# Kernel tuning notes

Measured on AMD Instinct MI355X. Metric: run time of the kernel, lower is better.

Reference implementation:

```python
import jax, jax.numpy as jnp
import numpy as np

EMB = 384
HEADS = 6
QDIM = 64
DFF = 4 * EMB
EPS = 1e-5


def layer_norm(x, g, b):
    mu = jnp.mean(x, axis=-1, keepdims=True)
    var = jnp.mean((x - mu) ** 2, axis=-1, keepdims=True)
    return (x - mu) * jax.lax.rsqrt(var + EPS) * g + b


def setup_inputs() -> dict:
    key = jax.random.key(0)
    ks = jax.random.split(key, 12)
    s = EMB ** -0.5
    return {
        "x": jax.random.normal(ks[0], (32, 512, EMB), dtype=jnp.float32),
        "Wq": jax.random.normal(ks[1], (EMB, EMB), dtype=jnp.float32) * s,
        "Wk": jax.random.normal(ks[2], (EMB, EMB), dtype=jnp.float32) * s,
        "Wv": jax.random.normal(ks[3], (EMB, EMB), dtype=jnp.float32) * s,
        "Wp": jax.random.normal(ks[4], (EMB, EMB), dtype=jnp.float32) * s,
        "bp": jnp.zeros((EMB,), dtype=jnp.float32),
        "g1": jnp.ones((EMB,), dtype=jnp.float32),
        "b1": jnp.zeros((EMB,), dtype=jnp.float32),
        "g2": jnp.ones((EMB,), dtype=jnp.float32),
        "b2": jnp.zeros((EMB,), dtype=jnp.float32),
        "W1": jax.random.normal(ks[5], (EMB, DFF), dtype=jnp.float32) * s,
        "bf1": jnp.zeros((DFF,), dtype=jnp.float32),
        "W2": jax.random.normal(ks[6], (DFF, EMB), dtype=jnp.float32) * (DFF ** -0.5),
        "bf2": jnp.zeros((EMB,), dtype=jnp.float32),
    }


def reference(x, Wq, Wk, Wv, Wp, bp, g1, b1, g2, b2, W1, bf1, W2, bf2):
    B, T, C = x.shape
    # --- self-attention on ln1(x) ---
    h = layer_norm(x, g1, b1)
    q = (h @ Wq).reshape(B, T, HEADS, QDIM).transpose(0, 2, 1, 3)  # [B,H,T,D]
    k = (h @ Wk).reshape(B, T, HEADS, QDIM).transpose(0, 2, 1, 3)
    v = (h @ Wv).reshape(B, T, HEADS, QDIM).transpose(0, 2, 1, 3)
    aff = jnp.einsum('bhtd,bhsd->bhts', q, k) * (QDIM ** -0.5)  # [B,H,T,T]
    causal = jnp.tril(jnp.ones((T, T), dtype=bool))
    aff = jnp.where(causal, aff, -jnp.inf)
    aff = jax.nn.softmax(aff, axis=-1)
    o = jnp.einsum('bhts,bhsd->bhtd', aff, v)
    o = o.transpose(0, 2, 1, 3).reshape(B, T, C)
    x = x + (o @ Wp + bp)
    # --- feed-forward on ln2(x) ---
    h2 = layer_norm(x, g2, b2)
    ff = jax.nn.relu(h2 @ W1 + bf1) @ W2 + bf2
    return x + ff
```

## Files before the change

kernel.cpp:

```cpp
#include <hip/hip_runtime.h>
#include <cstdint>
#include <cstddef>

#define DEVINL __device__ __forceinline__

typedef short short8 __attribute__((ext_vector_type(8)));
typedef float f32x4 __attribute__((ext_vector_type(4)));
typedef unsigned short ushort;
typedef ushort u16x8 __attribute__((ext_vector_type(8)));
typedef ushort u16x4 __attribute__((ext_vector_type(4)));

DEVINL float bf2f(ushort u) {
  union { unsigned int i; float f; } v; v.i = ((unsigned int)u) << 16; return v.f;
}
DEVINL ushort f2bf(float f) {
  union { float f; unsigned int i; } v; v.f = f;
  unsigned int u = v.i;
  unsigned int r = u + 0x7fffu + ((u >> 16) & 1u);
  return (ushort)(r >> 16);
}

DEVINL void gl2lds16(const ushort* g, ushort* l) {
  __builtin_amdgcn_global_load_lds(
      (const __attribute__((address_space(1))) void*)g,
      (__attribute__((address_space(3))) void*)l, 16, 0, 0);
}

__global__ void transpose6_k(const float* __restrict__ Wq, const float* __restrict__ Wk,
                             const float* __restrict__ Wv, const float* __restrict__ Wp,
                             const float* __restrict__ W1, const float* __restrict__ W2,
                             ushort* __restrict__ WqT, ushort* __restrict__ WkT,
                             ushort* __restrict__ WvT, ushort* __restrict__ WpT,
                             ushort* __restrict__ W1T, ushort* __restrict__ W2T) {
  __shared__ float tile[32][33];
  int z = blockIdx.z;
  const float* in;
  ushort* out;
  int R, C, bx, by;
  if (z < 4) {
    if (blockIdx.x >= 12) return;
    in = (z == 0) ? Wq : (z == 1) ? Wk : (z == 2) ? Wv : Wp;
    out = (z == 0) ? WqT : (z == 1) ? WkT : (z == 2) ? WvT : WpT;
    R = 384; C = 384; bx = blockIdx.x; by = blockIdx.y;
  } else if (z == 4) {
    in = W1; out = W1T; R = 384; C = 1536; bx = blockIdx.x; by = blockIdx.y;
  } else {
    in = W2; out = W2T; R = 1536; C = 384; bx = blockIdx.y; by = blockIdx.x;
  }
  int tx = threadIdx.x, ty = threadIdx.y;
  int x = bx * 32 + tx;
#pragma unroll
  for (int i = 0; i < 4; i++) {
    int y = by * 32 + ty + i * 8;
    tile[ty + i * 8][tx] = in[(size_t)y * C + x];
  }
  __syncthreads();
  int x2 = by * 32 + tx;
#pragma unroll
  for (int i = 0; i < 4; i++) {
    int y2 = bx * 32 + ty + i * 8;
    out[(size_t)y2 * R + x2] = f2bf(tile[tx][ty + i * 8]);
  }
}

__global__ __launch_bounds__(256) void ln_k(const float* __restrict__ x,
                                            const float* __restrict__ g,
                                            const float* __restrict__ b,
                                            ushort* __restrict__ out) {
  int wave = threadIdx.x >> 6;
  int lane = threadIdx.x & 63;
  int row = blockIdx.x * 4 + wave;
  const float* xr = x + (size_t)row * 384;
  float v[6];
#pragma unroll
  for (int j = 0; j < 3; j++) {
    float2 p = *(const float2*)(xr + lane * 2 + j * 128);
    v[2 * j] = p.x;
    v[2 * j + 1] = p.y;
  }
  float s = v[0] + v[1] + v[2] + v[3] + v[4] + v[5];
#pragma unroll
  for (int off = 32; off; off >>= 1) s += __shfl_xor(s, off);
  float mu = s * (1.0f / 384.0f);
  float s2 = 0.f;
#pragma unroll
  for (int j = 0; j < 6; j++) { float d = v[j] - mu; s2 += d * d; }
#pragma unroll
  for (int off = 32; off; off >>= 1) s2 += __shfl_xor(s2, off);
  float rs = rsqrtf(s2 * (1.0f / 384.0f) + 1e-5f);
  ushort* orow = out + (size_t)row * 384;
#pragma unroll
  for (int j = 0; j < 3; j++) {
    int c = lane * 2 + j * 128;
    float2 pg = *(const float2*)(g + c);
    float2 pb = *(const float2*)(b + c);
    float y0 = (v[2 * j] - mu) * rs * pg.x + pb.x;
    float y1 = (v[2 * j + 1] - mu) * rs * pg.y + pb.y;
    uint32_t po = (uint32_t)f2bf(y0) | ((uint32_t)f2bf(y1) << 16);
    *(uint32_t*)(orow + c) = po;
  }
}

template <int MODE, int TN>
__global__ __launch_bounds__(256) void gemm_k(
    const ushort* __restrict__ A, int K,
    const ushort* __restrict__ WTa, const ushort* __restrict__ WTb,
    const ushort* __restrict__ WTc,
    const float* __restrict__ bias, const float* residf,
    ushort* __restrict__ outa, ushort* __restrict__ outb,
    ushort* __restrict__ outc, float* outf) {
  constexpr int NJ = TN / 32;
  __shared__ __align__(16) ushort As[128 * 64];
  __shared__ __align__(16) ushort Bs[TN * 64];
  int tid = threadIdx.x;
  int lane = tid & 63, wave = tid >> 6;
  int wm = wave & 1, wn = wave >> 1;
  int q4 = lane >> 4, ln16 = lane & 15;
  int rowBase = blockIdx.x * 128;
  int colBase = blockIdx.y * TN;

  const ushort* WT;
  if (MODE == 0) {
    int z = blockIdx.z;
    WT = (z == 0) ? WTa : (z == 1) ? WTb : WTc;
  } else {
    WT = WTa;
  }

  f32x4 acc[4][NJ];
#pragma unroll
  for (int i = 0; i < 4; i++)
#pragma unroll
    for (int j = 0; j < NJ; j++) acc[i][j] = (f32x4){0.f, 0.f, 0.f, 0.f};

  int ri = lane >> 3;
  int g8 = (lane & 7) ^ ri;

  for (int kb = 0; kb < K; kb += 64) {
#pragma unroll
    for (int h = 0; h < 128; h += 32) {
      int base = h + wave * 8;
      gl2lds16(&A[(size_t)(rowBase + base + ri) * K + kb + g8 * 8], &As[base * 64]);
    }
#pragma unroll
    for (int h = 0; h < TN; h += 32) {
      int base = h + wave * 8;
      gl2lds16(&WT[(size_t)(colBase + base + ri) * K + kb + g8 * 8], &Bs[base * 64]);
    }
    __syncthreads();
#pragma unroll
    for (int ks = 0; ks < 2; ks++) {
      short8 af[4], bfr[NJ];
#pragma unroll
      for (int i = 0; i < 4; i++) {
        int ar = wm * 64 + i * 16 + ln16;
        int slot = (ks * 4 + q4) ^ (ar & 7);
        af[i] = *(const short8*)&As[ar * 64 + slot * 8];
      }
#pragma unroll
      for (int j = 0; j < NJ; j++) {
        int br = wn * (TN / 2) + j * 16 + ln16;
        int slot = (ks * 4 + q4) ^ (br & 7);
        bfr[j] = *(const short8*)&Bs[br * 64 + slot * 8];
      }
#pragma unroll
      for (int i = 0; i < 4; i++)
#pragma unroll
        for (int j = 0; j < NJ; j++)
          acc[i][j] = __builtin_amdgcn_mfma_f32_16x16x32_bf16(af[i], bfr[j], acc[i][j], 0, 0, 0);
    }
    __syncthreads();
  }

#pragma unroll
  for (int i = 0; i < 4; i++) {
#pragma unroll
    for (int j = 0; j < NJ; j++) {
      int row0 = rowBase + wm * 64 + i * 16 + q4 * 4;
      int col = colBase + wn * (TN / 2) + j * 16 + ln16;
      if (MODE == 0) {
        int z = blockIdx.z;
        if (z < 2) {
          float sc = (z == 0) ? 0.18033688011112f : 1.0f;
          ushort* o = (z == 0) ? outa : outb;
#pragma unroll
          for (int r = 0; r < 4; r++) {
            int row = row0 + r;
            int bb = row >> 9, t = row & 511, h = col >> 6, d = col & 63;
            o[(((size_t)(bb * 6 + h) * 512) + t) * 64 + d] = f2bf(acc[i][j][r] * sc);
          }
        } else {
          int bb = row0 >> 9, t0 = row0 & 511, h = col >> 6, d = col & 63;
          u16x4 pk = {f2bf(acc[i][j][0]), f2bf(acc[i][j][1]), f2bf(acc[i][j][2]),
                      f2bf(acc[i][j][3])};
          *(u16x4*)&outc[(((size_t)(bb * 6 + h) * 64) + d) * 512 + t0] = pk;
        }
      } else if (MODE == 1) {
        float bcol = bias[col];
#pragma unroll
        for (int r = 0; r < 4; r++) {
          size_t idx = (size_t)(row0 + r) * 384 + col;
          outf[idx] = acc[i][j][r] + bcol + residf[idx];
        }
      } else {
        float bcol = bias[col];
#pragma unroll
        for (int r = 0; r < 4; r++) {
          size_t idx = (size_t)(row0 + r) * 1536 + col;
          float vv = acc[i][j][r] + bcol;
          outa[idx] = f2bf(vv > 0.f ? vv : 0.f);
        }
      }
    }
  }
}

__global__ __launch_bounds__(256) void attn_k(const ushort* __restrict__ qg,
                                              const ushort* __restrict__ kg,
                                              const ushort* __restrict__ vtg,
                                              ushort* __restrict__ outg) {
  __shared__ __align__(16) ushort Ks[64 * 64];
  __shared__ __align__(16) ushort VTs[64 * 64];
  __shared__ __align__(16) ushort Pw[4][16][88];
  int tid = threadIdx.x, lane = tid & 63, wave = tid >> 6;
  int l = blockIdx.x;
  int xcd = l & 7, m = l >> 3;
  int bh = xcd * 24 + (m >> 2);
  int pr = m & 3;
  int lo = pr, hi = 7 - pr;
  int quad = lane >> 4, ln16 = lane & 15;
  int x7 = ln16 & 7;
  int slo = (quad ^ x7) * 8;
  int shi = slo ^ 32;

  const ushort* qp = qg + (size_t)bh * 512 * 64;
  const ushort* kp = kg + (size_t)bh * 512 * 64;
  const ushort* vp = vtg + (size_t)bh * 64 * 512;

  int ri = lane >> 3;
  int g8 = (lane & 7) ^ ri;

  int t_lo = lo * 64 + wave * 16 + ln16;
  int t_hi = hi * 64 + wave * 16 + ln16;
  short8 bqlo0 = *(const short8*)&qp[(size_t)t_lo * 64 + quad * 8];
  short8 bqlo1 = *(const short8*)&qp[(size_t)t_lo * 64 + 32 + quad * 8];
  short8 bqhi0 = *(const short8*)&qp[(size_t)t_hi * 64 + quad * 8];
  short8 bqhi1 = *(const short8*)&qp[(size_t)t_hi * 64 + 32 + quad * 8];

  f32x4 Olo[4], Ohi[4];
#pragma unroll
  for (int dt = 0; dt < 4; dt++) {
    Olo[dt] = (f32x4){0.f, 0.f, 0.f, 0.f};
    Ohi[dt] = (f32x4){0.f, 0.f, 0.f, 0.f};
  }
  float m_lo = -3.0e38f, l_lo = 0.f, m_hi = -3.0e38f, l_hi = 0.f;

  auto process = [&](short8 q0f, short8 q1f, int t_row, float& m_, float& l_,
                     f32x4* O, int s0, bool maskit) {
    f32x4 St[4];
    __builtin_amdgcn_s_setprio(1);
#pragma unroll
    for (int kt = 0; kt < 4; kt++) {
      int r = kt * 16 + ln16;
      short8 a0 = *(const short8*)&Ks[r * 64 + slo];
      short8 a1 = *(const short8*)&Ks[r * 64 + shi];
      f32x4 z = (f32x4){0.f, 0.f, 0.f, 0.f};
      z = __builtin_amdgcn_mfma_f32_16x16x32_bf16(a0, q0f, z, 0, 0, 0);
      z = __builtin_amdgcn_mfma_f32_16x16x32_bf16(a1, q1f, z, 0, 0, 0);
      St[kt] = z;
    }
    __builtin_amdgcn_s_setprio(0);
    if (maskit) {
#pragma unroll
      for (int kt = 0; kt < 4; kt++)
#pragma unroll
        for (int r = 0; r < 4; r++) {
          int s_abs = s0 + kt * 16 + quad * 4 + r;
          St[kt][r] = (s_abs <= t_row) ? St[kt][r] : -3.0e38f;
        }
    }
    float vm = St[0][0];
#pragma unroll
    for (int kt = 0; kt < 4; kt++)
#pragma unroll
      for (int r = 0; r < 4; r++) vm = fmaxf(vm, St[kt][r]);
    vm = fmaxf(vm, __shfl_xor(vm, 16));
    vm = fmaxf(vm, __shfl_xor(vm, 32));
    float mn = fmaxf(m_, vm);
    if (!__all(mn - m_ <= 8.0f)) {
      float alpha = exp2f(m_ - mn);
      m_ = mn;
      l_ *= alpha;
#pragma unroll
      for (int dt = 0; dt < 4; dt++)
#pragma unroll
        for (int r = 0; r < 4; r++) O[dt][r] *= alpha;
    }
    float ps = 0.f;
#pragma unroll
    for (int kt = 0; kt < 4; kt++)
#pragma unroll
      for (int r = 0; r < 4; r++) {
        float p = exp2f(St[kt][r] - m_);
        St[kt][r] = p;
        ps += p;
      }
    ps += __shfl_xor(ps, 16);
    ps += __shfl_xor(ps, 32);
    l_ += ps;

    asm volatile("" ::: "memory");
#pragma unroll
    for (int kt = 0; kt < 4; kt++) {
      u16x4 pk = {f2bf(St[kt][0]), f2bf(St[kt][1]), f2bf(St[kt][2]), f2bf(St[kt][3])};
      *(u16x4*)&Pw[wave][ln16][kt * 16 + quad * 4] = pk;
    }
    asm volatile("" ::: "memory");
    union { u16x8 u; short8 s; } p0, p1;
    p0.u = *(const u16x8*)&Pw[wave][ln16][quad * 8];
    p1.u = *(const u16x8*)&Pw[wave][ln16][32 + quad * 8];
    __builtin_amdgcn_s_setprio(1);
#pragma unroll
    for (int dt = 0; dt < 4; dt++) {
      int r = dt * 16 + ln16;
      short8 v0 = *(const short8*)&VTs[r * 64 + slo];
      short8 v1 = *(const short8*)&VTs[r * 64 + shi];
      O[dt] = __builtin_amdgcn_mfma_f32_16x16x32_bf16(v0, p0.s, O[dt], 0, 0, 0);
      O[dt] = __builtin_amdgcn_mfma_f32_16x16x32_bf16(v1, p1.s, O[dt], 0, 0, 0);
    }
    __builtin_amdgcn_s_setprio(0);
  };

  for (int s0 = 0; s0 <= hi * 64; s0 += 64) {
#pragma unroll
    for (int h = 0; h < 64; h += 32) {
      int base = h + wave * 8;
      gl2lds16(&kp[(size_t)(s0 + base + ri) * 64 + g8 * 8], &Ks[base * 64]);
      gl2lds16(&vp[(size_t)(base + ri) * 512 + s0 + g8 * 8], &VTs[base * 64]);
    }
    __syncthreads();
    if (s0 <= lo * 64) process(bqlo0, bqlo1, t_lo, m_lo, l_lo, Olo, s0, s0 == lo * 64);
    process(bqhi0, bqhi1, t_hi, m_hi, l_hi, Ohi, s0, s0 == hi * 64);
    __syncthreads();
  }

  int b = bh / 6, h = bh % 6;
  float ilo = 1.0f / l_lo, ihi = 1.0f / l_hi;
  size_t base_lo = ((size_t)(b * 512) + t_lo) * 384 + h * 64;
  size_t base_hi = ((size_t)(b * 512) + t_hi) * 384 + h * 64;
#pragma unroll
  for (int dt = 0; dt < 4; dt++) {
    u16x4 plo = {f2bf(Olo[dt][0] * ilo), f2bf(Olo[dt][1] * ilo),
                 f2bf(Olo[dt][2] * ilo), f2bf(Olo[dt][3] * ilo)};
    *(u16x4*)&outg[base_lo + dt * 16 + quad * 4] = plo;
    u16x4 phi = {f2bf(Ohi[dt][0] * ihi), f2bf(Ohi[dt][1] * ihi),
                 f2bf(Ohi[dt][2] * ihi), f2bf(Ohi[dt][3] * ihi)};
    *(u16x4*)&outg[base_hi + dt * 16 + quad * 4] = phi;
  }
}

extern "C" void kernel_launch(void* const* d_in, const int* in_sizes, int n_in,
                              void* d_out, int out_size, void* d_ws, size_t ws_size,
                              hipStream_t stream) {
  const float* x = (const float*)d_in[0];
  const float* Wq = (const float*)d_in[1];
  const float* Wk = (const float*)d_in[2];
  const float* Wv = (const float*)d_in[3];
  const float* Wp = (const float*)d_in[4];
  const float* bp = (const float*)d_in[5];
  const float* g1 = (const float*)d_in[6];
  const float* b1 = (const float*)d_in[7];
  const float* g2 = (const float*)d_in[8];
  const float* b2 = (const float*)d_in[9];
  const float* W1 = (const float*)d_in[10];
  const float* bf1 = (const float*)d_in[11];
  const float* W2 = (const float*)d_in[12];
  const float* bf2 = (const float*)d_in[13];
  float* outp = (float*)d_out;

  char* ws = (char*)d_ws;
  size_t off = 0;
  auto alloc = [&](size_t elems) {
    ushort* p = (ushort*)(ws + off);
    off += elems * 2;
    return p;
  };
  ushort* WqT = alloc((size_t)384 * 384);
  ushort* WkT = alloc((size_t)384 * 384);
  ushort* WvT = alloc((size_t)384 * 384);
  ushort* WpT = alloc((size_t)384 * 384);
  ushort* W1T = alloc((size_t)384 * 1536);
  ushort* W2T = alloc((size_t)1536 * 384);
  ushort* bufq = alloc((size_t)16384 * 384);
  ushort* m1 = alloc((size_t)16384 * 1536);
  ushort* h1_attn = m1;
  ushort* bufk = m1 + (size_t)16384 * 384;
  ushort* vT = m1 + (size_t)2 * 16384 * 384;

  dim3 tb(32, 8);
  transpose6_k<<<dim3(48, 12, 6), tb, 0, stream>>>(Wq, Wk, Wv, Wp, W1, W2,
                                                   WqT, WkT, WvT, WpT, W1T, W2T);

  ln_k<<<4096, 256, 0, stream>>>(x, g1, b1, h1_attn);
  gemm_k<0, 128><<<dim3(128, 3, 3), 256, 0, stream>>>(
      h1_attn, 384, WqT, WkT, WvT, nullptr, nullptr, bufq, bufk, vT, nullptr);
  attn_k<<<768, 256, 0, stream>>>(bufq, bufk, vT, h1_attn);
  gemm_k<1, 64><<<dim3(128, 6), 256, 0, stream>>>(
      h1_attn, 384, WpT, nullptr, nullptr, bp, x, nullptr, nullptr, nullptr, outp);
  ln_k<<<4096, 256, 0, stream>>>(outp, g2, b2, bufq);
  gemm_k<2, 128><<<dim3(128, 12), 256, 0, stream>>>(
      bufq, 384, W1T, nullptr, nullptr, bf1, nullptr, m1, nullptr, nullptr, nullptr);
  gemm_k<1, 64><<<dim3(128, 6), 256, 0, stream>>>(
      m1, 1536, W2T, nullptr, nullptr, bf2, outp, nullptr, nullptr, nullptr, outp);
}
```

Measured before the change: 248.0 us.

## Fuse second LayerNorm into output-projection GEMM epilogue with full-row tiles

Adds a gemmrow_k kernel whose tile is 64 rows by all 384 output columns, so each block holds complete rows. The epilogue adds bias and residual, writes the fp32 result, and for the projection GEMM also computes LN2 statistics with shuffles plus an LDS reduction and writes the bf16 normalized activations. This removes the separate ln_k launch and its re-read of the fp32 residual stream. The W2 down-projection also moves to this kernel, but only 256 blocks of 512 threads launch with no double buffering, which may underuse the GPU compared with the earlier 768-block grid.

```diff
diff --git a/kernel.cpp b/kernel.cpp
--- a/kernel.cpp
+++ b/kernel.cpp
@@ -106,9 +106,9 @@
     const ushort* __restrict__ A, int K,
     const ushort* __restrict__ WTa, const ushort* __restrict__ WTb,
     const ushort* __restrict__ WTc,
-    const float* __restrict__ bias, const float* residf,
+    const float* __restrict__ bias,
     ushort* __restrict__ outa, ushort* __restrict__ outb,
-    ushort* __restrict__ outc, float* outf) {
+    ushort* __restrict__ outc) {
   constexpr int NJ = TN / 32;
   __shared__ __align__(16) ushort As[128 * 64];
   __shared__ __align__(16) ushort Bs[TN * 64];
@@ -195,13 +195,6 @@
                       f2bf(acc[i][j][3])};
           *(u16x4*)&outc[(((size_t)(bb * 6 + h) * 64) + d) * 512 + t0] = pk;
         }
-      } else if (MODE == 1) {
-        float bcol = bias[col];
-#pragma unroll
-        for (int r = 0; r < 4; r++) {
-          size_t idx = (size_t)(row0 + r) * 384 + col;
-          outf[idx] = acc[i][j][r] + bcol + residf[idx];
-        }
       } else {
         float bcol = bias[col];
 #pragma unroll
@@ -209,6 +202,127 @@
           size_t idx = (size_t)(row0 + r) * 1536 + col;
           float vv = acc[i][j][r] + bcol;
           outa[idx] = f2bf(vv > 0.f ? vv : 0.f);
+        }
+      }
+    }
+  }
+}
+
+template <int EPI>
+__global__ __launch_bounds__(512, 4) void gemmrow_k(
+    const ushort* __restrict__ A, int K, const ushort* __restrict__ WT,
+    const float* __restrict__ bias, const float* __restrict__ residf,
+    const float* __restrict__ g, const float* __restrict__ bln,
+    float* __restrict__ outf, ushort* __restrict__ outh) {
+  __shared__ __align__(16) ushort As[64 * 64];
+  __shared__ __align__(16) ushort Bs[384 * 64];
+  int tid = threadIdx.x;
+  int lane = tid & 63, wave = tid >> 6;
+  int wm = wave & 1, wn = wave >> 1;
+  int q4 = lane >> 4, ln16 = lane & 15;
+  int rowBase = blockIdx.x * 64;
+
+  f32x4 acc[2][6];
+#pragma unroll
+  for (int i = 0; i < 2; i++)
+#pragma unroll
+    for (int j = 0; j < 6; j++) acc[i][j] = (f32x4){0.f, 0.f, 0.f, 0.f};
+
+  int ri = lane >> 3;
+  int g8 = (lane & 7) ^ ri;
+
+  for (int kb = 0; kb < K; kb += 64) {
+    gl2lds16(&A[(size_t)(rowBase + wave * 8 + ri) * K + kb + g8 * 8],
+             &As[(wave * 8) * 64]);
+#pragma unroll
+    for (int s = 0; s < 6; s++) {
+      int base = s * 64 + wave * 8;
+      gl2lds16(&WT[(size_t)(base + ri) * K + kb + g8 * 8], &Bs[base * 64]);
+    }
+    __syncthreads();
+#pragma unroll
+    for (int ks = 0; ks < 2; ks++) {
+      short8 af[2], bfr[6];
+#pragma unroll
+      for (int i = 0; i < 2; i++) {
+        int ar = wm * 32 + i * 16 + ln16;
+        int slot = (ks * 4 + q4) ^ (ar & 7);
+        af[i] = *(const short8*)&As[ar * 64 + slot * 8];
+      }
+#pragma unroll
+      for (int j = 0; j < 6; j++) {
+        int br = wn * 96 + j * 16 + ln16;
+        int slot = (ks * 4 + q4) ^ (br & 7);
+        bfr[j] = *(const short8*)&Bs[br * 64 + slot * 8];
+      }
+#pragma unroll
+      for (int i = 0; i < 2; i++)
+#pragma unroll
+        for (int j = 0; j < 6; j++)
+          acc[i][j] = __builtin_amdgcn_mfma_f32_16x16x32_bf16(af[i], bfr[j], acc[i][j], 0, 0, 0);
+    }
+    __syncthreads();
+  }
+
+  float s1[2][4], s2v[2][4];
+#pragma unroll
+  for (int i = 0; i < 2; i++)
+#pragma unroll
+    for (int r = 0; r < 4; r++) { s1[i][r] = 0.f; s2v[i][r] = 0.f; }
+
+#pragma unroll
+  for (int i = 0; i < 2; i++) {
+#pragma unroll
+    for (int j = 0; j < 6; j++) {
+      int col = wn * 96 + j * 16 + ln16;
+      float bcol = bias[col];
+      int row0 = rowBase + wm * 32 + i * 16 + q4 * 4;
+#pragma unroll
+      for (int r = 0; r < 4; r++) {
+        size_t idx = (size_t)(row0 + r) * 384 + col;
+        float val = acc[i][j][r] + bcol + residf[idx];
+        outf[idx] = val;
+        acc[i][j][r] = val;
+        if (EPI == 0) { s1[i][r] += val; s2v[i][r] += val * val; }
+      }
+    }
+  }
+
+  if (EPI == 0) {
+    float* red = (float*)As;
+#pragma unroll
+    for (int i = 0; i < 2; i++)
+#pragma unroll
+      for (int r = 0; r < 4; r++) {
+        float a = s1[i][r], b = s2v[i][r];
+#pragma unroll
+        for (int m = 1; m <= 8; m <<= 1) {
+          a += __shfl_xor(a, m);
+          b += __shfl_xor(b, m);
+        }
+        if (ln16 == 0) {
+          int lr = wm * 32 + i * 16 + q4 * 4 + r;
+          red[wn * 64 + lr] = a;
+          red[256 + wn * 64 + lr] = b;
+        }
+      }
+    __syncthreads();
+#pragma unroll
+    for (int i = 0; i < 2; i++) {
+#pragma unroll
+      for (int r = 0; r < 4; r++) {
+        int lr = wm * 32 + i * 16 + q4 * 4 + r;
+        float a = red[lr] + red[64 + lr] + red[128 + lr] + red[192 + lr];
+        float b = red[256 + lr] + red[320 + lr] + red[448 - 64 + lr] + red[448 + lr];
+        float mu = a * (1.0f / 384.0f);
+        float var = b * (1.0f / 384.0f) - mu * mu;
+        float rs = rsqrtf(var + 1e-5f);
+        int row = rowBase + lr;
+#pragma unroll
+        for (int j = 0; j < 6; j++) {
+          int col = wn * 96 + j * 16 + ln16;
+          float hv = (acc[i][j][r] - mu) * rs * g[col] + bln[col];
+          outh[(size_t)row * 384 + col] = f2bf(hv);
         }
       }
     }
@@ -403,13 +517,12 @@
 
   ln_k<<<4096, 256, 0, stream>>>(x, g1, b1, h1_attn);
   gemm_k<0, 128><<<dim3(128, 3, 3), 256, 0, stream>>>(
-      h1_attn, 384, WqT, WkT, WvT, nullptr, nullptr, bufq, bufk, vT, nullptr);
+      h1_attn, 384, WqT, WkT, WvT, nullptr, bufq, bufk, vT);
   attn_k<<<768, 256, 0, stream>>>(bufq, bufk, vT, h1_attn);
-  gemm_k<1, 64><<<dim3(128, 6), 256, 0, stream>>>(
-      h1_attn, 384, WpT, nullptr, nullptr, bp, x, nullptr, nullptr, nullptr, outp);
-  ln_k<<<4096, 256, 0, stream>>>(outp, g2, b2, bufq);
+  gemmrow_k<0><<<256, 512, 0, stream>>>(
+      h1_attn, 384, WpT, bp, x, g2, b2, outp, bufq);
   gemm_k<2, 128><<<dim3(128, 12), 256, 0, stream>>>(
-      bufq, 384, W1T, nullptr, nullptr, bf1, nullptr, m1, nullptr, nullptr, nullptr);
-  gemm_k<1, 64><<<dim3(128, 6), 256, 0, stream>>>(
-      m1, 1536, W2T, nullptr, nullptr, bf2, outp, nullptr, nullptr, nullptr, outp);
-}
+      bufq, 384, W1T, nullptr, nullptr, bf1, m1, nullptr, nullptr);
+  gemmrow_k<1><<<256, 512, 0, stream>>>(
+      m1, 1536, W2T, bf2, outp, nullptr, nullptr, outp, nullptr);
+}
```

Result: slower. 255.8 us (+3.1%).

## Double-buffer K/V tiles in attention kernel to overlap loads with MFMA

Applied to the files above, without the earlier changes.

The attention kernel now keeps two LDS buffers for K and V^T tiles and issues the global-to-LDS loads for the next tile before computing the current one. A partial vmcnt wait lets the next tile's loads stay in flight while the current tile is processed. This targets the stall where each iteration waited for its loads to finish before any compute could start. In exchange LDS use roughly doubles, which may lower occupancy, and correctness now depends on the hand-written vmcnt counts and barriers.

```diff
diff --git a/kernel.cpp b/kernel.cpp
--- a/kernel.cpp
+++ b/kernel.cpp
@@ -219,8 +219,8 @@
                                               const ushort* __restrict__ kg,
                                               const ushort* __restrict__ vtg,
                                               ushort* __restrict__ outg) {
-  __shared__ __align__(16) ushort Ks[64 * 64];
-  __shared__ __align__(16) ushort VTs[64 * 64];
+  __shared__ __align__(16) ushort Ks[2][64 * 64];
+  __shared__ __align__(16) ushort VTs[2][64 * 64];
   __shared__ __align__(16) ushort Pw[4][16][88];
   int tid = threadIdx.x, lane = tid & 63, wave = tid >> 6;
   int l = blockIdx.x;
@@ -255,15 +255,25 @@
   }
   float m_lo = -3.0e38f, l_lo = 0.f, m_hi = -3.0e38f, l_hi = 0.f;
 
+  auto STAGEKV = [&](int buf, int s0) {
+#pragma unroll
+    for (int h = 0; h < 64; h += 32) {
+      int base = h + wave * 8;
+      gl2lds16(&kp[(size_t)(s0 + base + ri) * 64 + g8 * 8], &Ks[buf][base * 64]);
+      gl2lds16(&vp[(size_t)(base + ri) * 512 + s0 + g8 * 8], &VTs[buf][base * 64]);
+    }
+  };
+
   auto process = [&](short8 q0f, short8 q1f, int t_row, float& m_, float& l_,
-                     f32x4* O, int s0, bool maskit) {
+                     f32x4* O, int s0, bool maskit,
+                     const ushort* Kb, const ushort* Vb) {
     f32x4 St[4];
     __builtin_amdgcn_s_setprio(1);
 #pragma unroll
     for (int kt = 0; kt < 4; kt++) {
       int r = kt * 16 + ln16;
-      short8 a0 = *(const short8*)&Ks[r * 64 + slo];
-      short8 a1 = *(const short8*)&Ks[r * 64 + shi];
+      short8 a0 = *(const short8*)&Kb[r * 64 + slo];
+      short8 a1 = *(const short8*)&Kb[r * 64 + shi];
       f32x4 z = (f32x4){0.f, 0.f, 0.f, 0.f};
       z = __builtin_amdgcn_mfma_f32_16x16x32_bf16(a0, q0f, z, 0, 0, 0);
       z = __builtin_amdgcn_mfma_f32_16x16x32_bf16(a1, q1f, z, 0, 0, 0);
@@ -323,25 +333,35 @@
 #pragma unroll
     for (int dt = 0; dt < 4; dt++) {
       int r = dt * 16 + ln16;
-      short8 v0 = *(const short8*)&VTs[r * 64 + slo];
-      short8 v1 = *(const short8*)&VTs[r * 64 + shi];
+      short8 v0 = *(const short8*)&Vb[r * 64 + slo];
+      short8 v1 = *(const short8*)&Vb[r * 64 + shi];
       O[dt] = __builtin_amdgcn_mfma_f32_16x16x32_bf16(v0, p0.s, O[dt], 0, 0, 0);
       O[dt] = __builtin_amdgcn_mfma_f32_16x16x32_bf16(v1, p1.s, O[dt], 0, 0, 0);
     }
     __builtin_amdgcn_s_setprio(0);
   };
 
-  for (int s0 = 0; s0 <= hi * 64; s0 += 64) {
-#pragma unroll
-    for (int h = 0; h < 64; h += 32) {
-      int base = h + wave * 8;
-      gl2lds16(&kp[(size_t)(s0 + base + ri) * 64 + g8 * 8], &Ks[base * 64]);
-      gl2lds16(&vp[(size_t)(base + ri) * 512 + s0 + g8 * 8], &VTs[base * 64]);
-    }
-    __syncthreads();
-    if (s0 <= lo * 64) process(bqlo0, bqlo1, t_lo, m_lo, l_lo, Olo, s0, s0 == lo * 64);
-    process(bqhi0, bqhi1, t_hi, m_hi, l_hi, Ohi, s0, s0 == hi * 64);
-    __syncthreads();
+  int nt = hi + 1;
+  STAGEKV(0, 0);
+  for (int t = 0; t < nt; ++t) {
+    int cur = t & 1;
+    if (t + 1 < nt) {
+      STAGEKV(cur ^ 1, (t + 1) << 6);
+      asm volatile("s_waitcnt vmcnt(4)" ::: "memory");
+    } else {
+      asm volatile("s_waitcnt vmcnt(0)" ::: "memory");
+    }
+    __builtin_amdgcn_sched_barrier(0);
+    __builtin_amdgcn_s_barrier();
+    __builtin_amdgcn_sched_barrier(0);
+    int s0 = t << 6;
+    if (s0 <= lo * 64)
+      process(bqlo0, bqlo1, t_lo, m_lo, l_lo, Olo, s0, s0 == lo * 64,
+              &Ks[cur][0], &VTs[cur][0]);
+    process(bqhi0, bqhi1, t_hi, m_hi, l_hi, Ohi, s0, s0 == hi * 64,
+            &Ks[cur][0], &VTs[cur][0]);
+    __builtin_amdgcn_sched_barrier(0);
+    __builtin_amdgcn_s_barrier();
   }
 
   int b = bh / 6, h = bh % 6;
```

Measured after the change: 248.0 us (median of 2 runs). No clear change (-0.0%).
